# Kernel tuning notes

Hardware: AMD Instinct MI355X
Metric: run time of the kernel (lower is better)

## Reference

```python
import jax, jax.numpy as jnp
import numpy as np

N_NODES = 50000
N_EDGES = 800000
N_GRAPHS = 64


def _gcn_conv(h, src, dst, norm, w, b, n):
    # h: [N, Fin]; src/dst: [E+N] (self-loops appended); norm: [E+N]
    h = h @ w  # [N, Fout]
    msg = h[src] * norm[:, None]  # gather + degree-normalize
    out = jax.ops.segment_sum(msg, dst, num_segments=n)  # scatter-add
    return out + b


def setup_inputs() -> dict:
    key = jax.random.key(0)
    ks = jax.random.split(key, 8)
    x = jax.random.normal(ks[0], (N_NODES, 128), dtype=jnp.float32)
    edge_index = jax.random.randint(ks[1], (2, N_EDGES), 0, N_NODES, dtype=jnp.int64)
    batch = jnp.sort(jax.random.randint(ks[2], (N_NODES,), 0, N_GRAPHS, dtype=jnp.int64))
    conv_w = jax.random.normal(ks[3], (3, 128, 128), dtype=jnp.float32) * (1.0 / np.sqrt(128))
    conv_b = jnp.zeros((3, 128), dtype=jnp.float32)
    lin1_w = jax.random.normal(ks[4], (384, 128), dtype=jnp.float32) * (1.0 / np.sqrt(384))
    lin1_b = jnp.zeros((128,), dtype=jnp.float32)
    lin2_w = jax.random.normal(ks[5], (128, 2), dtype=jnp.float32) * (1.0 / np.sqrt(128))
    lin2_b = jnp.zeros((2,), dtype=jnp.float32)
    return dict(x=x, edge_index=edge_index, batch=batch, conv_w=conv_w, conv_b=conv_b,
                lin1_w=lin1_w, lin1_b=lin1_b, lin2_w=lin2_w, lin2_b=lin2_b)


def reference(x, edge_index, batch, conv_w, conv_b, lin1_w, lin1_b, lin2_w, lin2_b):
    n = x.shape[0]
    loop = jnp.arange(n, dtype=edge_index.dtype)
    src = jnp.concatenate([edge_index[0], loop])  # add self-loops (PyG GCNConv default)
    dst = jnp.concatenate([edge_index[1], loop])
    deg = jax.ops.segment_sum(jnp.ones_like(dst, dtype=x.dtype), dst, num_segments=n)
    dinv = jnp.where(deg > 0, jax.lax.rsqrt(deg), 0.0)
    norm = dinv[src] * dinv[dst]  # symmetric normalization D^-1/2 A D^-1/2

    h = x
    for l in range(conv_w.shape[0]):
        h = jax.nn.relu(_gcn_conv(h, src, dst, norm, conv_w[l], conv_b[l], n))

    addp = jax.ops.segment_sum(h, batch, num_segments=N_GRAPHS)
    cnt = jax.ops.segment_sum(jnp.ones((n,), dtype=h.dtype), batch, num_segments=N_GRAPHS)
    meanp = addp / jnp.maximum(cnt, 1.0)[:, None]
    maxp = jax.ops.segment_max(h, batch, num_segments=N_GRAPHS)
    enc = jnp.concatenate([addp, meanp, maxp], axis=1)  # [G, 3*hidden]

    out = jax.nn.relu(enc @ lin1_w + lin1_b) @ lin2_w + lin2_b
    return out, enc
```

## Files before the change

kernel.cpp:

```cpp
#include <hip/hip_runtime.h>

#define NN 50000
#define NE 800000
#define NG 64
#define FD 128
#define SCAN_NB ((NN + 255) / 256)
#define NROLE 8
#define NCHUNK 98
#define NODES_PER_ROLE (NN / NROLE)

typedef unsigned int uint;
typedef unsigned short ushort;
typedef __attribute__((ext_vector_type(8))) short short8v;
typedef __attribute__((ext_vector_type(4))) float f32x4;

__device__ __forceinline__ uint pack2bf(float a, float b) {
  uint ua = __float_as_uint(a);
  uint ub = __float_as_uint(b);
  ua = (ua + 0x7fffu + ((ua >> 16) & 1u)) >> 16;
  ub = (ub + 0x7fffu + ((ub >> 16) & 1u)) >> 16;
  return ua | (ub << 16);
}

__device__ __forceinline__ ushort bf16of(float v) {
  uint u = __float_as_uint(v);
  u = (u + 0x7fffu + ((u >> 16) & 1u)) >> 16;
  return (ushort)u;
}

#define BFLO(u) __uint_as_float((u) << 16)
#define BFHI(u) __uint_as_float((u) & 0xffff0000u)


__global__ void k_zwp(const float* __restrict__ conv_w, uint* __restrict__ w16,
                      int* __restrict__ indeg, float* __restrict__ addp,
                      float* __restrict__ cnt, uint* __restrict__ maxp) {
  int gtid = blockIdx.x * 256 + threadIdx.x;
  if (gtid < NN) indeg[gtid] = 0;
  if (gtid < NG * FD) { addp[gtid] = 0.f; maxp[gtid] = 0u; }
  if (gtid < NG) cnt[gtid] = 0.f;
  if (gtid < 96 * 64) {
    int id = gtid >> 6, l = gtid & 63;
    int layer = id >> 5, t = (id >> 3) & 3, nt = id & 7;
    const float* W = conv_w + layer * FD * FD;
    int col = nt * 16 + (l & 15);
    int k0 = t * 32 + 8 * (l >> 4);
    uint4 u;
    u.x = pack2bf(W[(k0 + 0) * FD + col], W[(k0 + 1) * FD + col]);
    u.y = pack2bf(W[(k0 + 2) * FD + col], W[(k0 + 3) * FD + col]);
    u.z = pack2bf(W[(k0 + 4) * FD + col], W[(k0 + 5) * FD + col]);
    u.w = pack2bf(W[(k0 + 6) * FD + col], W[(k0 + 7) * FD + col]);
    ((uint4*)w16)[id * 64 + l] = u;
  }
}


__global__ void k_count(const int* __restrict__ dst, int* __restrict__ indeg) {
  int role = blockIdx.x & (NROLE - 1);
  int chunk = blockIdx.x >> 3;
  int lo = role * NODES_PER_ROLE, hi = lo + NODES_PER_ROLE;
  for (int i = chunk * 256 + threadIdx.x; i < NE / 4; i += NCHUNK * 256) {
    int4 d = ((const int4*)dst)[i];
    if (d.x >= lo && d.x < hi) atomicAdd(&indeg[d.x], 1);
    if (d.y >= lo && d.y < hi) atomicAdd(&indeg[d.y], 1);
    if (d.z >= lo && d.z < hi) atomicAdd(&indeg[d.z], 1);
    if (d.w >= lo && d.w < hi) atomicAdd(&indeg[d.w], 1);
  }
}

__global__ void k_scan1(const int* __restrict__ indeg, int* __restrict__ locpre,
                        int* __restrict__ blocksum) {
  __shared__ int sums[256];
  int t = threadIdx.x;
  int idx = blockIdx.x * 256 + t;
  int v = (idx < NN) ? indeg[idx] : 0;
  sums[t] = v;
  __syncthreads();
  for (int off = 1; off < 256; off <<= 1) {
    int u = (t >= off) ? sums[t - off] : 0;
    __syncthreads();
    sums[t] += u;
    __syncthreads();
  }
  if (idx < NN) locpre[idx] = sums[t] - v;
  if (t == 255) blocksum[blockIdx.x] = sums[255];
}

__global__ void k_scan2(int* __restrict__ blocksum, int* __restrict__ blockoff,
                        int* __restrict__ row_off) {
  __shared__ int sums[256];
  int t = threadIdx.x;
  int v = (t < SCAN_NB) ? blocksum[t] : 0;
  sums[t] = v;
  __syncthreads();
  for (int off = 1; off < 256; off <<= 1) {
    int u = (t >= off) ? sums[t - off] : 0;
    __syncthreads();
    sums[t] += u;
    __syncthreads();
  }
  if (t < SCAN_NB) blockoff[t] = sums[t] - v;
  if (t == 255) row_off[NN] = sums[255];
}

__global__ void k_scan3(const int* __restrict__ indeg, const int* __restrict__ locpre,
                        const int* __restrict__ blockoff, int* __restrict__ row_off,
                        float* __restrict__ dinv, int* __restrict__ cursor) {
  int idx = blockIdx.x * 256 + threadIdx.x;
  if (idx < NN) {
    int ro = blockoff[blockIdx.x] + locpre[idx];
    row_off[idx] = ro;
    cursor[idx] = ro;
    dinv[idx] = rsqrtf((float)(indeg[idx] + 1));
  }
}

__global__ void k_fill(const int* __restrict__ src, const int* __restrict__ dst,
                       int* __restrict__ cursor, int* __restrict__ csr_src) {
  int role = blockIdx.x & (NROLE - 1);
  int chunk = blockIdx.x >> 3;
  int lo = role * NODES_PER_ROLE, hi = lo + NODES_PER_ROLE;
  for (int i = chunk * 256 + threadIdx.x; i < NE / 4; i += NCHUNK * 256) {
    int4 s = ((const int4*)src)[i];
    int4 d = ((const int4*)dst)[i];
    if (d.x >= lo && d.x < hi) { int p = atomicAdd(&cursor[d.x], 1); csr_src[p] = s.x; }
    if (d.y >= lo && d.y < hi) { int p = atomicAdd(&cursor[d.y], 1); csr_src[p] = s.y; }
    if (d.z >= lo && d.z < hi) { int p = atomicAdd(&cursor[d.z], 1); csr_src[p] = s.z; }
    if (d.w >= lo && d.w < hi) { int p = atomicAdd(&cursor[d.w], 1); csr_src[p] = s.w; }
  }
}


__device__ __forceinline__ uint4 agg_node(const uint* __restrict__ gin,
                                          const int* __restrict__ row_off,
                                          const int* __restrict__ csr_src,
                                          const float* __restrict__ dinv,
                                          const float* __restrict__ bias,
                                          int node, int lane) {
  const uint4* gp = (const uint4*)gin;
  float a[8];
  uint4 sv = gp[(size_t)node * 16 + lane];
  a[0] = BFLO(sv.x); a[1] = BFHI(sv.x);
  a[2] = BFLO(sv.y); a[3] = BFHI(sv.y);
  a[4] = BFLO(sv.z); a[5] = BFHI(sv.z);
  a[6] = BFLO(sv.w); a[7] = BFHI(sv.w);

#define ACC8(v)                                      \
  a[0] += BFLO(v.x); a[1] += BFHI(v.x);              \
  a[2] += BFLO(v.y); a[3] += BFHI(v.y);              \
  a[4] += BFLO(v.z); a[5] += BFHI(v.z);              \
  a[6] += BFLO(v.w); a[7] += BFHI(v.w);

  int e0 = row_off[node], e1 = row_off[node + 1];
  int e = e0;
  for (; e + 4 <= e1; e += 4) {
    int s0 = csr_src[e + 0];
    int s1 = csr_src[e + 1];
    int s2 = csr_src[e + 2];
    int s3 = csr_src[e + 3];
    uint4 v0 = gp[(size_t)s0 * 16 + lane];
    uint4 v1 = gp[(size_t)s1 * 16 + lane];
    uint4 v2 = gp[(size_t)s2 * 16 + lane];
    uint4 v3 = gp[(size_t)s3 * 16 + lane];
    ACC8(v0) ACC8(v1) ACC8(v2) ACC8(v3)
  }
  for (; e < e1; ++e) {
    int s = csr_src[e];
    uint4 v = gp[(size_t)s * 16 + lane];
    ACC8(v)
  }
#undef ACC8

  float d = dinv[node];
  int f0 = lane * 8;
  float4 b1 = *(const float4*)(bias + f0);
  float4 b2 = *(const float4*)(bias + f0 + 4);
  float o0 = fmaxf(fmaf(d, a[0], b1.x), 0.f);
  float o1 = fmaxf(fmaf(d, a[1], b1.y), 0.f);
  float o2 = fmaxf(fmaf(d, a[2], b1.z), 0.f);
  float o3 = fmaxf(fmaf(d, a[3], b1.w), 0.f);
  float o4 = fmaxf(fmaf(d, a[4], b2.x), 0.f);
  float o5 = fmaxf(fmaf(d, a[5], b2.y), 0.f);
  float o6 = fmaxf(fmaf(d, a[6], b2.z), 0.f);
  float o7 = fmaxf(fmaf(d, a[7], b2.w), 0.f);
  uint4 ov;
  ov.x = pack2bf(o0, o1);
  ov.y = pack2bf(o2, o3);
  ov.z = pack2bf(o4, o5);
  ov.w = pack2bf(o6, o7);
  return ov;
}


__global__ __launch_bounds__(256) void k_aggmm(const uint* __restrict__ gin,
                                               const int* __restrict__ row_off,
                                               const int* __restrict__ csr_src,
                                               const float* __restrict__ dinv,
                                               const float* __restrict__ bias,
                                               const uint* __restrict__ wfrag,
                                               uint* __restrict__ gout) {
  __shared__ uint hs[16][68];
  int tid = threadIdx.x;
  int n = tid >> 4, lane = tid & 15;
  int node = blockIdx.x * 16 + n;
  uint4 ov = agg_node(gin, row_off, csr_src, dinv, bias, node, lane);
  *(uint4*)&hs[n][lane * 4] = ov;
  __syncthreads();

  int wv = tid >> 6, l = tid & 63;
  int lr = l & 15, lg = l >> 4;
  const uint4* wl = (const uint4*)wfrag;
  f32x4 acc[2] = {};
#pragma unroll
  for (int t = 0; t < 4; ++t) {
    uint4 a4 = *(const uint4*)&hs[lr][t * 16 + 4 * lg];
    short8v av = __builtin_bit_cast(short8v, a4);
#pragma unroll
    for (int q = 0; q < 2; ++q) {
      int nt = wv * 2 + q;
      uint4 b = wl[(t * 8 + nt) * 64 + l];
      short8v bv = __builtin_bit_cast(short8v, b);
      acc[q] = __builtin_amdgcn_mfma_f32_16x16x32_bf16(av, bv, acc[q], 0, 0, 0);
    }
  }
  int row0 = blockIdx.x * 16;
  ushort* gp_out = (ushort*)gout;
#pragma unroll
  for (int r = 0; r < 4; ++r) {
    int row = row0 + 4 * lg + r;
    float d = dinv[row];
#pragma unroll
    for (int q = 0; q < 2; ++q) {
      int nt = wv * 2 + q;
      gp_out[(size_t)row * FD + nt * 16 + lr] = bf16of(acc[q][r] * d);
    }
  }
}


__global__ __launch_bounds__(256) void k_aggpool(const uint* __restrict__ gin,
                                                 const int* __restrict__ row_off,
                                                 const int* __restrict__ csr_src,
                                                 const float* __restrict__ dinv,
                                                 const float* __restrict__ bias,
                                                 const int* __restrict__ batch,
                                                 float* __restrict__ addp,
                                                 float* __restrict__ cnt,
                                                 uint* __restrict__ maxp) {
  __shared__ uint hs[16][68];
  int tid = threadIdx.x;
  int n = tid >> 4, lane = tid & 15;
  int node = blockIdx.x * 16 + n;
  uint4 ov = agg_node(gin, row_off, csr_src, dinv, bias, node, lane);
  *(uint4*)&hs[n][lane * 4] = ov;
  __syncthreads();

  if (tid < 64) {
    int f = tid;
    int n0 = blockIdx.x * 16;
    int curg = batch[n0];
    float s0 = 0.f, s1 = 0.f, m0 = 0.f, m1 = 0.f;
    int c = 0;
    for (int k = 0; k < 16; ++k) {
      int gi = batch[n0 + k];
      if (gi != curg) {
        atomicAdd(&addp[curg * FD + 2 * f], s0);
        atomicAdd(&addp[curg * FD + 2 * f + 1], s1);
        atomicMax(&maxp[curg * FD + 2 * f], __float_as_uint(m0));
        atomicMax(&maxp[curg * FD + 2 * f + 1], __float_as_uint(m1));
        if (f == 0) atomicAdd(&cnt[curg], (float)c);
        s0 = 0.f; s1 = 0.f; m0 = 0.f; m1 = 0.f; c = 0; curg = gi;
      }
      uint u = hs[k][f];
      float lo = BFLO(u), hi = BFHI(u);
      s0 += lo; s1 += hi;
      m0 = fmaxf(m0, lo); m1 = fmaxf(m1, hi);
      c += 1;
    }
    atomicAdd(&addp[curg * FD + 2 * f], s0);
    atomicAdd(&addp[curg * FD + 2 * f + 1], s1);
    atomicMax(&maxp[curg * FD + 2 * f], __float_as_uint(m0));
    atomicMax(&maxp[curg * FD + 2 * f + 1], __float_as_uint(m1));
    if (f == 0) atomicAdd(&cnt[curg], (float)c);
  }
}


__global__ __launch_bounds__(256) void k_mm_f32(const float* __restrict__ x,
                                                const uint* __restrict__ wfrag,
                                                const float* __restrict__ dinv,
                                                uint* __restrict__ g16) {
  int tid = threadIdx.x;
  int wv = tid >> 6, l = tid & 63;
  int lr = l & 15, lg = l >> 4;
  int row0 = blockIdx.x * 64 + wv * 16;
  const uint4* wl = (const uint4*)wfrag;
  int arow = row0 + lr; if (arow > NN - 1) arow = NN - 1;
  const float* xrow = x + (size_t)arow * FD;
  f32x4 acc[8] = {};
#pragma unroll 2
  for (int t = 0; t < 4; ++t) {
    float4 p = *(const float4*)(xrow + t * 32 + 8 * lg);
    float4 q = *(const float4*)(xrow + t * 32 + 8 * lg + 4);
    uint4 a;
    a.x = pack2bf(p.x, p.y); a.y = pack2bf(p.z, p.w);
    a.z = pack2bf(q.x, q.y); a.w = pack2bf(q.z, q.w);
    short8v av = __builtin_bit_cast(short8v, a);
#pragma unroll
    for (int nt = 0; nt < 8; ++nt) {
      uint4 b = wl[(t * 8 + nt) * 64 + l];
      short8v bv = __builtin_bit_cast(short8v, b);
      acc[nt] = __builtin_amdgcn_mfma_f32_16x16x32_bf16(av, bv, acc[nt], 0, 0, 0);
    }
  }
  ushort* gout = (ushort*)g16;
#pragma unroll
  for (int r = 0; r < 4; ++r) {
    int row = row0 + 4 * lg + r;
    bool ok = row < NN;
    float d = dinv[ok ? row : 0];
#pragma unroll
    for (int nt = 0; nt < 8; ++nt) {
      if (ok) gout[(size_t)row * FD + nt * 16 + lr] = bf16of(acc[nt][r] * d);
    }
  }
}


__global__ void k_final(const float* __restrict__ addp, const float* __restrict__ cnt,
                        const unsigned int* __restrict__ maxp,
                        const float* __restrict__ l1w, const float* __restrict__ l1b,
                        const float* __restrict__ l2w, const float* __restrict__ l2b,
                        float* __restrict__ d_out) {
  __shared__ float enc_s[384];
  __shared__ float hid_s[128];
  int gph = blockIdx.x, j = threadIdx.x;
  float a = addp[gph * FD + j];
  float c = cnt[gph];
  float mn = a / fmaxf(c, 1.f);
  float mx = __uint_as_float(maxp[gph * FD + j]);
  enc_s[j] = a; enc_s[128 + j] = mn; enc_s[256 + j] = mx;
  float* enc_out = d_out + 2 * NG;
  enc_out[gph * 384 + j] = a;
  enc_out[gph * 384 + 128 + j] = mn;
  enc_out[gph * 384 + 256 + j] = mx;
  __syncthreads();
  float sacc = l1b[j];
  for (int k = 0; k < 384; ++k) sacc = fmaf(enc_s[k], l1w[k * FD + j], sacc);
  hid_s[j] = fmaxf(sacc, 0.f);
  __syncthreads();
  if (j < 2) {
    float o = l2b[j];
    for (int k = 0; k < FD; ++k) o = fmaf(hid_s[k], l2w[k * 2 + j], o);
    d_out[gph * 2 + j] = o;
  }
}

extern "C" void kernel_launch(void* const* d_in, const int* in_sizes, int n_in,
                              void* d_out, int out_size, void* d_ws, size_t ws_size,
                              hipStream_t stream) {
  const float* x      = (const float*)d_in[0];
  const int*   edge   = (const int*)d_in[1];
  const int*   batch  = (const int*)d_in[2];
  const float* conv_w = (const float*)d_in[3];
  const float* conv_b = (const float*)d_in[4];
  const float* l1w    = (const float*)d_in[5];
  const float* l1b    = (const float*)d_in[6];
  const float* l2w    = (const float*)d_in[7];
  const float* l2b    = (const float*)d_in[8];
  float* out = (float*)d_out;

  const int* esrc = edge;
  const int* edst = edge + NE;

  char* wsp = (char*)d_ws;
  auto alloc = [&](size_t bytes) -> char* {
    char* p = wsp;
    wsp += (bytes + 255) & ~(size_t)255;
    return p;
  };
  uint*  gbufA   = (uint*)alloc(2u * NN * FD);
  uint*  gbufB   = (uint*)alloc(2u * NN * FD);
  uint*  w16     = (uint*)alloc(2u * 3 * FD * FD);
  int*   csr_src = (int*)alloc(sizeof(int) * NE);
  int*   indeg   = (int*)alloc(sizeof(int) * NN);
  int*   row_off = (int*)alloc(sizeof(int) * (NN + 1));
  int*   cursor  = (int*)alloc(sizeof(int) * NN);
  int*   locpre  = (int*)alloc(sizeof(int) * NN);
  int*   blocksum= (int*)alloc(sizeof(int) * SCAN_NB);
  int*   blockoff= (int*)alloc(sizeof(int) * SCAN_NB);
  float* dinv    = (float*)alloc(sizeof(float) * NN);
  float* addp    = (float*)alloc(sizeof(float) * NG * FD);
  float* cnt     = (float*)alloc(sizeof(float) * NG);
  unsigned int* maxp = (unsigned int*)alloc(sizeof(unsigned int) * NG * FD);

  k_zwp<<<(NN + 255) / 256, 256, 0, stream>>>(conv_w, w16, indeg, addp, cnt, maxp);
  k_count<<<NROLE * NCHUNK, 256, 0, stream>>>(edst, indeg);
  k_scan1<<<SCAN_NB, 256, 0, stream>>>(indeg, locpre, blocksum);
  k_scan2<<<1, 256, 0, stream>>>(blocksum, blockoff, row_off);
  k_scan3<<<SCAN_NB, 256, 0, stream>>>(indeg, locpre, blockoff, row_off, dinv, cursor);
  k_fill<<<NROLE * NCHUNK, 256, 0, stream>>>(esrc, edst, cursor, csr_src);

  const int WBLK = FD * FD / 2;
  k_mm_f32<<<(NN + 63) / 64, 256, 0, stream>>>(x, w16, dinv, gbufA);
  k_aggmm<<<NN / 16, 256, 0, stream>>>(gbufA, row_off, csr_src, dinv,
                                       conv_b + 0 * FD, w16 + 1 * WBLK, gbufB);
  k_aggmm<<<NN / 16, 256, 0, stream>>>(gbufB, row_off, csr_src, dinv,
                                       conv_b + 1 * FD, w16 + 2 * WBLK, gbufA);
  k_aggpool<<<NN / 16, 256, 0, stream>>>(gbufA, row_off, csr_src, dinv,
                                         conv_b + 2 * FD, batch, addp, cnt, maxp);
  k_final<<<NG, 128, 0, stream>>>(addp, cnt, maxp, l1w, l1b, l2w, l2b, out);
}
```

Measured before the change: 231.0 us.

## Split each node's edge aggregation across two half-warps and widen blocks to 512

```diff
diff --git a/kernel.cpp b/kernel.cpp
--- a/kernel.cpp
+++ b/kernel.cpp
@@ -131,45 +131,68 @@
 }
 
 
-__device__ __forceinline__ uint4 agg_node(const uint* __restrict__ gin,
-                                          const int* __restrict__ row_off,
-                                          const int* __restrict__ csr_src,
-                                          const float* __restrict__ dinv,
-                                          const float* __restrict__ bias,
-                                          int node, int lane) {
+__device__ __forceinline__ uint4 agg_node32(const uint* __restrict__ gin,
+                                            const int* __restrict__ row_off,
+                                            const int* __restrict__ csr_src,
+                                            const float* __restrict__ dinv,
+                                            const float* __restrict__ bias,
+                                            int node, int lane32) {
+  int half = lane32 >> 4, lane = lane32 & 15;
   const uint4* gp = (const uint4*)gin;
-  float a[8];
-  uint4 sv = gp[(size_t)node * 16 + lane];
-  a[0] = BFLO(sv.x); a[1] = BFHI(sv.x);
-  a[2] = BFLO(sv.y); a[3] = BFHI(sv.y);
-  a[4] = BFLO(sv.z); a[5] = BFHI(sv.z);
-  a[6] = BFLO(sv.w); a[7] = BFHI(sv.w);
-
-#define ACC8(v)                                      \
-  a[0] += BFLO(v.x); a[1] += BFHI(v.x);              \
-  a[2] += BFLO(v.y); a[3] += BFHI(v.y);              \
-  a[4] += BFLO(v.z); a[5] += BFHI(v.z);              \
-  a[6] += BFLO(v.w); a[7] += BFHI(v.w);
+  float a[8] = {}, b[8] = {};
+  if (half == 0) {
+    uint4 sv = gp[(size_t)node * 16 + lane];
+    a[0] = BFLO(sv.x); a[1] = BFHI(sv.x);
+    a[2] = BFLO(sv.y); a[3] = BFHI(sv.y);
+    a[4] = BFLO(sv.z); a[5] = BFHI(sv.z);
+    a[6] = BFLO(sv.w); a[7] = BFHI(sv.w);
+  }
+
+#define ACC8(acc, v)                                       \
+  acc[0] += BFLO(v.x); acc[1] += BFHI(v.x);                \
+  acc[2] += BFLO(v.y); acc[3] += BFHI(v.y);                \
+  acc[4] += BFLO(v.z); acc[5] += BFHI(v.z);                \
+  acc[6] += BFLO(v.w); acc[7] += BFHI(v.w);
 
   int e0 = row_off[node], e1 = row_off[node + 1];
-  int e = e0;
-  for (; e + 4 <= e1; e += 4) {
-    int s0 = csr_src[e + 0];
-    int s1 = csr_src[e + 1];
-    int s2 = csr_src[e + 2];
-    int s3 = csr_src[e + 3];
+  int deg = e1 - e0;
+  int m = e0 + ((deg + 1) >> 1);
+  int e = half ? m : e0;
+  int end = half ? e1 : m;
+  for (; e + 8 <= end; e += 8) {
+    int s0 = csr_src[e + 0], s1 = csr_src[e + 1];
+    int s2 = csr_src[e + 2], s3 = csr_src[e + 3];
+    int s4 = csr_src[e + 4], s5 = csr_src[e + 5];
+    int s6 = csr_src[e + 6], s7 = csr_src[e + 7];
     uint4 v0 = gp[(size_t)s0 * 16 + lane];
     uint4 v1 = gp[(size_t)s1 * 16 + lane];
     uint4 v2 = gp[(size_t)s2 * 16 + lane];
     uint4 v3 = gp[(size_t)s3 * 16 + lane];
-    ACC8(v0) ACC8(v1) ACC8(v2) ACC8(v3)
-  }
-  for (; e < e1; ++e) {
+    uint4 v4 = gp[(size_t)s4 * 16 + lane];
+    uint4 v5 = gp[(size_t)s5 * 16 + lane];
+    uint4 v6 = gp[(size_t)s6 * 16 + lane];
+    uint4 v7 = gp[(size_t)s7 * 16 + lane];
+    ACC8(a, v0) ACC8(b, v1) ACC8(a, v2) ACC8(b, v3)
+    ACC8(a, v4) ACC8(b, v5) ACC8(a, v6) ACC8(b, v7)
+  }
+  for (; e + 2 <= end; e += 2) {
+    int s0 = csr_src[e + 0], s1 = csr_src[e + 1];
+    uint4 v0 = gp[(size_t)s0 * 16 + lane];
+    uint4 v1 = gp[(size_t)s1 * 16 + lane];
+    ACC8(a, v0) ACC8(b, v1)
+  }
+  if (e < end) {
     int s = csr_src[e];
     uint4 v = gp[(size_t)s * 16 + lane];
-    ACC8(v)
+    ACC8(a, v)
   }
 #undef ACC8
+
+#pragma unroll
+  for (int j = 0; j < 8; ++j) {
+    a[j] += b[j];
+    a[j] += __shfl_xor(a[j], 16);
+  }
 
   float d = dinv[node];
   int f0 = lane * 8;
@@ -192,7 +215,7 @@
 }
 
 
-__global__ __launch_bounds__(256) void k_aggmm(const uint* __restrict__ gin,
+__global__ __launch_bounds__(512) void k_aggmm(const uint* __restrict__ gin,
                                                const int* __restrict__ row_off,
                                                const int* __restrict__ csr_src,
                                                const float* __restrict__ dinv,
@@ -201,27 +224,23 @@
                                                uint* __restrict__ gout) {
   __shared__ uint hs[16][68];
   int tid = threadIdx.x;
-  int n = tid >> 4, lane = tid & 15;
+  int n = tid >> 5, lane32 = tid & 31;
   int node = blockIdx.x * 16 + n;
-  uint4 ov = agg_node(gin, row_off, csr_src, dinv, bias, node, lane);
-  *(uint4*)&hs[n][lane * 4] = ov;
+  uint4 ov = agg_node32(gin, row_off, csr_src, dinv, bias, node, lane32);
+  if (lane32 < 16) *(uint4*)&hs[n][lane32 * 4] = ov;
   __syncthreads();
 
   int wv = tid >> 6, l = tid & 63;
   int lr = l & 15, lg = l >> 4;
   const uint4* wl = (const uint4*)wfrag;
-  f32x4 acc[2] = {};
+  f32x4 acc = {};
 #pragma unroll
   for (int t = 0; t < 4; ++t) {
     uint4 a4 = *(const uint4*)&hs[lr][t * 16 + 4 * lg];
     short8v av = __builtin_bit_cast(short8v, a4);
-#pragma unroll
-    for (int q = 0; q < 2; ++q) {
-      int nt = wv * 2 + q;
-      uint4 b = wl[(t * 8 + nt) * 64 + l];
-      short8v bv = __builtin_bit_cast(short8v, b);
-      acc[q] = __builtin_amdgcn_mfma_f32_16x16x32_bf16(av, bv, acc[q], 0, 0, 0);
-    }
+    uint4 b4 = wl[(t * 8 + wv) * 64 + l];
+    short8v bv = __builtin_bit_cast(short8v, b4);
+    acc = __builtin_amdgcn_mfma_f32_16x16x32_bf16(av, bv, acc, 0, 0, 0);
   }
   int row0 = blockIdx.x * 16;
   ushort* gp_out = (ushort*)gout;
@@ -229,16 +248,12 @@
   for (int r = 0; r < 4; ++r) {
     int row = row0 + 4 * lg + r;
     float d = dinv[row];
-#pragma unroll
-    for (int q = 0; q < 2; ++q) {
-      int nt = wv * 2 + q;
-      gp_out[(size_t)row * FD + nt * 16 + lr] = bf16of(acc[q][r] * d);
-    }
-  }
-}
-
-
-__global__ __launch_bounds__(256) void k_aggpool(const uint* __restrict__ gin,
+    gp_out[(size_t)row * FD + wv * 16 + lr] = bf16of(acc[r] * d);
+  }
+}
+
+
+__global__ __launch_bounds__(512) void k_aggpool(const uint* __restrict__ gin,
                                                  const int* __restrict__ row_off,
                                                  const int* __restrict__ csr_src,
                                                  const float* __restrict__ dinv,
@@ -249,10 +264,10 @@
                                                  uint* __restrict__ maxp) {
   __shared__ uint hs[16][68];
   int tid = threadIdx.x;
-  int n = tid >> 4, lane = tid & 15;
+  int n = tid >> 5, lane32 = tid & 31;
   int node = blockIdx.x * 16 + n;
-  uint4 ov = agg_node(gin, row_off, csr_src, dinv, bias, node, lane);
-  *(uint4*)&hs[n][lane * 4] = ov;
+  uint4 ov = agg_node32(gin, row_off, csr_src, dinv, bias, node, lane32);
+  if (lane32 < 16) *(uint4*)&hs[n][lane32 * 4] = ov;
   __syncthreads();
 
   if (tid < 64) {
@@ -403,11 +418,11 @@
 
   const int WBLK = FD * FD / 2;
   k_mm_f32<<<(NN + 63) / 64, 256, 0, stream>>>(x, w16, dinv, gbufA);
-  k_aggmm<<<NN / 16, 256, 0, stream>>>(gbufA, row_off, csr_src, dinv,
+  k_aggmm<<<NN / 16, 512, 0, stream>>>(gbufA, row_off, csr_src, dinv,
                                        conv_b + 0 * FD, w16 + 1 * WBLK, gbufB);
-  k_aggmm<<<NN / 16, 256, 0, stream>>>(gbufB, row_off, csr_src, dinv,
+  k_aggmm<<<NN / 16, 512, 0, stream>>>(gbufB, row_off, csr_src, dinv,
                                        conv_b + 1 * FD, w16 + 2 * WBLK, gbufA);
-  k_aggpool<<<NN / 16, 256, 0, stream>>>(gbufA, row_off, csr_src, dinv,
+  k_aggpool<<<NN / 16, 512, 0, stream>>>(gbufA, row_off, csr_src, dinv,
                                          conv_b + 2 * FD, batch, addp, cnt, maxp);
   k_final<<<NG, 128, 0, stream>>>(addp, cnt, maxp, l1w, l1b, l2w, l2b, out);
 }
```

Result: slower. 268.8 us (+16.4%).
